# Kernel optimization log

Measured on AMD Instinct MI355X. Metric: run time of the kernel, lower is better.

The kernel has to match this reference:

```python
import jax, jax.numpy as jnp
import numpy as np

NUM_EXPERTS = 8
TOP_K = 2


def setup_inputs() -> dict:
    key = jax.random.key(0)
    ks = jax.random.split(key, 6)
    B, S, D, H, E = 4, 1024, 1024, 2048, NUM_EXPERTS
    x = jax.random.normal(ks[0], (B, S, D), dtype=jnp.float32)
    Wg = jax.random.normal(ks[1], (D, E), dtype=jnp.float32) * 0.02
    W1 = jax.random.normal(ks[2], (E, D, H), dtype=jnp.float32) * 0.02
    b1 = jax.random.normal(ks[3], (E, H), dtype=jnp.float32) * 0.02
    W2 = jax.random.normal(ks[4], (E, H, D), dtype=jnp.float32) * 0.02
    b2 = jax.random.normal(ks[5], (E, D), dtype=jnp.float32) * 0.02
    return {"x": x, "Wg": Wg, "W1": W1, "b1": b1, "W2": W2, "b2": b2}


def reference(x, Wg, W1, b1, W2, b2):
    B, S, D = x.shape
    E, _, H = W1.shape
    OUT = W2.shape[2]
    xm = x.reshape(-1, D)                      # [N, D], N = B*S
    # --- top-k gating (ProbabilitySamplerTopk): softmax over experts, take top-k ---
    logits = xm @ Wg                           # [N, E]
    probs = jax.nn.softmax(logits, axis=-1)
    topk_p, topk_i = jax.lax.top_k(probs, TOP_K)   # [N, K]
    # --- sort dispatched (token, expert) pairs by expert id (stable) ---
    flat_e = topk_i.reshape(-1)                # [N*K]
    flat_p = topk_p.reshape(-1)                # [N*K]
    order = jnp.argsort(flat_e)                # stable sort -> grouped by expert
    tok_idx = order // TOP_K                   # source token index (trunc-div by topK)
    e_sorted = flat_e[order]                   # [N*K]
    p_sorted = flat_p[order]                   # [N*K]
    xs = xm[tok_idx]                           # [N*K, D] expert-sorted inputs
    # --- grouped-GEMM experts: masked per-expert dense GEMM (E is small & fixed) ---
    y = jnp.zeros((xs.shape[0], OUT), dtype=xs.dtype)
    for e in range(E):
        h = jax.nn.relu(xs @ W1[e] + b1[e])    # [N*K, H]
        ye = h @ W2[e] + b2[e]                 # [N*K, OUT]
        m = (e_sorted == e)[:, None].astype(xs.dtype)
        y = y + m * ye
    # --- combine: multiply by gates, scatter-add back to token slots ---
    y = y * p_sorted[:, None]
    out = jnp.zeros((B * S, OUT), dtype=y.dtype).at[tok_idx].add(y)
    return out.reshape(B, S, OUT)
```

## Files before the change

### kernel.cpp

```cpp
#include <hip/hip_runtime.h>
#include <hip/hip_bf16.h>
#include <stdint.h>

typedef __bf16 bf16;
typedef __bf16 bf16x8 __attribute__((ext_vector_type(8)));
typedef __bf16 bf16x4 __attribute__((ext_vector_type(4)));
typedef float f32x4 __attribute__((ext_vector_type(4)));

#define N_TOK 4096
#define DDIM 1024
#define HDIM 2048
#define NPAIR 8192
#define BM 128
#define BN 128
#define BK 32
#define MTILES 71

__device__ __forceinline__ void gload16(const void* g, void* l) {
  __builtin_amdgcn_global_load_lds(
      (const __attribute__((address_space(1))) unsigned int*)g,
      (__attribute__((address_space(3))) unsigned int*)l, 16, 0, 0);
}

__global__ void transpose_cvt_kernel(const float* __restrict__ in, bf16* __restrict__ out,
                                     int R, int C) {
  __shared__ float tile[32][33];
  const float* ip = in + (size_t)blockIdx.z * R * C;
  bf16* op = out + (size_t)blockIdx.z * R * C;
  int r0 = blockIdx.y * 32, c0 = blockIdx.x * 32;
  int tr = threadIdx.x >> 3;
  int tc = (threadIdx.x & 7) * 4;
  float4 v = *(const float4*)(ip + (size_t)(r0 + tr) * C + c0 + tc);
  tile[tr][tc] = v.x; tile[tr][tc + 1] = v.y; tile[tr][tc + 2] = v.z; tile[tr][tc + 3] = v.w;
  __syncthreads();
  bf16x4 o = {(bf16)tile[tc + 0][tr], (bf16)tile[tc + 1][tr],
              (bf16)tile[tc + 2][tr], (bf16)tile[tc + 3][tr]};
  *(bf16x4*)(op + (size_t)(c0 + tr) * R + r0 + tc) = o;
}

__global__ void gate_kernel(const float* __restrict__ x, const float* __restrict__ Wg,
                            int2* __restrict__ ge, float2* __restrict__ gp,
                            bf16* __restrict__ xb) {
  int t = blockIdx.x * 4 + (threadIdx.x >> 6);
  int lane = threadIdx.x & 63;
  const float* xr = x + (size_t)t * DDIM;
  bf16* xbr = xb + (size_t)t * DDIM;
  float a[8];
#pragma unroll
  for (int e = 0; e < 8; e++) a[e] = 0.f;
#pragma unroll
  for (int it = 0; it < 4; it++) {
    int d0 = it * 256 + lane * 4;
    float4 xv = *(const float4*)(xr + d0);
    bf16x4 o = {(bf16)xv.x, (bf16)xv.y, (bf16)xv.z, (bf16)xv.w};
    *(bf16x4*)(xbr + d0) = o;
    float xs[4] = {xv.x, xv.y, xv.z, xv.w};
#pragma unroll
    for (int dd = 0; dd < 4; dd++) {
      float4 w0 = *(const float4*)(Wg + (size_t)(d0 + dd) * 8);
      float4 w1 = *(const float4*)(Wg + (size_t)(d0 + dd) * 8 + 4);
      a[0] += xs[dd] * w0.x; a[1] += xs[dd] * w0.y; a[2] += xs[dd] * w0.z; a[3] += xs[dd] * w0.w;
      a[4] += xs[dd] * w1.x; a[5] += xs[dd] * w1.y; a[6] += xs[dd] * w1.z; a[7] += xs[dd] * w1.w;
    }
  }
#pragma unroll
  for (int off = 32; off >= 1; off >>= 1) {
#pragma unroll
    for (int e = 0; e < 8; e++) a[e] += __shfl_xor(a[e], off);
  }
  if (lane == 0) {
    float m = a[0];
#pragma unroll
    for (int e = 1; e < 8; e++) m = fmaxf(m, a[e]);
    float p[8]; float s = 0.f;
#pragma unroll
    for (int e = 0; e < 8; e++) { p[e] = expf(a[e] - m); s += p[e]; }
    float inv = 1.f / s;
    int i0 = 0; float v0 = a[0];
#pragma unroll
    for (int e = 1; e < 8; e++) if (a[e] > v0) { v0 = a[e]; i0 = e; }
    int i1 = -1; float v1 = -1e30f;
#pragma unroll
    for (int e = 0; e < 8; e++) if (e != i0 && a[e] > v1) { v1 = a[e]; i1 = e; }
    ge[t] = make_int2(i0, i1);
    gp[t] = make_float2(p[i0] * inv, p[i1] * inv);
  }
}

__global__ void sort_kernel(const int2* __restrict__ ge, const float2* __restrict__ gp,
                            int* __restrict__ tok, float* __restrict__ ps,
                            int* __restrict__ pairpos, int* __restrict__ meta) {
  __shared__ int hist[8], runn[8], wc[16][8], wb[16][8], baseS[9];
  int tid = threadIdx.x;
  int lane = tid & 63, wv = tid >> 6;
  if (tid < 8) hist[tid] = 0;
  __syncthreads();
  for (int i = tid; i < NPAIR; i += 1024) {
    int2 g = ge[i >> 1];
    int e = (i & 1) ? g.y : g.x;
    atomicAdd(&hist[e], 1);
  }
  __syncthreads();
  if (tid == 0) {
    int b = 0, ts = 0;
    for (int e = 0; e < 8; e++) {
      baseS[e] = b; meta[e] = b; meta[9 + e] = ts;
      b += hist[e]; ts += (hist[e] + BM - 1) / BM;
    }
    baseS[8] = b; meta[8] = b; meta[17] = ts;
  }
  __syncthreads();
  if (tid < 8) runn[tid] = baseS[tid];
  __syncthreads();
  for (int c = 0; c < 8; c++) {
    int i = c * 1024 + tid;
    int2 g = ge[i >> 1];
    int e = (i & 1) ? g.y : g.x;
    int rank = 0;
#pragma unroll
    for (int ee = 0; ee < 8; ee++) {
      unsigned long long b = __ballot(e == ee);
      if (e == ee) rank = __popcll(b & ((1ull << lane) - 1ull));
      if (lane == 0) wc[wv][ee] = __popcll(b);
    }
    __syncthreads();
    if (tid < 8) {
      int s = runn[tid];
      for (int w = 0; w < 16; w++) { wb[w][tid] = s; s += wc[w][tid]; }
      runn[tid] = s;
    }
    __syncthreads();
    int pos = wb[wv][e] + rank;
    tok[pos] = i >> 1;
    float2 p2 = gp[i >> 1];
    ps[pos] = (i & 1) ? p2.y : p2.x;
    pairpos[i] = pos;
    __syncthreads();
  }
}

template <int KDIM, int NPE, bool FIRST>
__global__ __launch_bounds__(256, 3)
void moe_gemm_kernel(const bf16* __restrict__ A, const bf16* __restrict__ Bt,
                     const float* __restrict__ bias, const int* __restrict__ tok,
                     const float* __restrict__ ps, const int* __restrict__ meta,
                     bf16* __restrict__ hout, float* __restrict__ y2, int MT) {
  __shared__ bf16 lds[3][8192];

  int nwg = gridDim.x;
  int orig = blockIdx.x;
  int q = nwg >> 3, rr8 = nwg & 7;
  int xcd = orig & 7, off8 = orig >> 3;
  int lin = (xcd < rr8 ? xcd * (q + 1) : rr8 * (q + 1) + (xcd - rr8) * q) + off8;
  int tileN = lin / MT;
  int tileM = lin - tileN * MT;
  if (tileM >= meta[17]) return;
  int e = 0;
#pragma unroll
  for (int k = 1; k < 8; k++) if (tileM >= meta[9 + k]) e = k;
  int row0 = meta[e] + (tileM - meta[9 + e]) * BM;
  int segEnd = meta[e + 1];
  int n0 = tileN * BN;

  int t = threadIdx.x;
  const bf16* aSrc[2];
  const bf16* bSrc[2];
#pragma unroll
  for (int r = 0; r < 2; r++) {
    int row = r * 64 + (t >> 2);
    int gRow = row0 + row; if (gRow > NPAIR - 1) gRow = NPAIR - 1;
    int arow = FIRST ? tok[gRow] : gRow;
    int gcol = ((t & 3) ^ ((row >> 1) & 3)) * 8;
    aSrc[r] = A + (size_t)arow * KDIM + gcol;
    bSrc[r] = Bt + ((size_t)e * NPE + n0 + row) * KDIM + gcol;
  }

  int lane = t & 63, wv = t >> 6;
  int wm = wv >> 1, wn = wv & 1;
  int l15 = lane & 15, l4 = lane >> 4;
  int aOff[4], bOff[4];
#pragma unroll
  for (int m = 0; m < 4; m++) {
    int row = wm * 64 + m * 16 + l15;
    aOff[m] = row * 32 + ((l4 ^ ((row >> 1) & 3)) * 8);
  }
#pragma unroll
  for (int n = 0; n < 4; n++) {
    int row = wn * 64 + n * 16 + l15;
    bOff[n] = 4096 + row * 32 + ((l4 ^ ((row >> 1) & 3)) * 8);
  }

  f32x4 acc[4][4];
#pragma unroll
  for (int m = 0; m < 4; m++)
#pragma unroll
    for (int n = 0; n < 4; n++)
#pragma unroll
      for (int j = 0; j < 4; j++) acc[m][n][j] = 0.f;

  auto STAGE = [&](int kt, int slot) {
    bf16* sb = &lds[slot][0];
    int ko = kt * BK;
    gload16(aSrc[0] + ko, sb + t * 8);
    gload16(aSrc[1] + ko, sb + 2048 + t * 8);
    gload16(bSrc[0] + ko, sb + 4096 + t * 8);
    gload16(bSrc[1] + ko, sb + 6144 + t * 8);
  };

  constexpr int nk = KDIM / BK;
  STAGE(0, 0);
  STAGE(1, 1);
  for (int kt = 0; kt < nk; kt++) {
    if (kt == nk - 1) asm volatile("s_waitcnt vmcnt(0)\n\ts_barrier" ::: "memory");
    else              asm volatile("s_waitcnt vmcnt(4)\n\ts_barrier" ::: "memory");
    if (kt + 2 < nk) STAGE(kt + 2, (kt + 2) % 3);
    __builtin_amdgcn_sched_barrier(0);
    const bf16* sb = &lds[kt % 3][0];
    bf16x8 af[4], bfr[4];
#pragma unroll
    for (int m = 0; m < 4; m++) af[m] = *(const bf16x8*)(sb + aOff[m]);
#pragma unroll
    for (int n = 0; n < 4; n++) bfr[n] = *(const bf16x8*)(sb + bOff[n]);
    __builtin_amdgcn_s_setprio(1);
#pragma unroll
    for (int m = 0; m < 4; m++)
#pragma unroll
      for (int n = 0; n < 4; n++)
        acc[m][n] = __builtin_amdgcn_mfma_f32_16x16x32_bf16(af[m], bfr[n], acc[m][n], 0, 0, 0);
    __builtin_amdgcn_s_setprio(0);
  }

  int colb = n0 + wn * 64 + l15;
  int rowb = wm * 64 + l4 * 4;
  float bia[4];
#pragma unroll
  for (int n = 0; n < 4; n++) bia[n] = bias[(size_t)e * NPE + colb + n * 16];
#pragma unroll
  for (int m = 0; m < 4; m++) {
#pragma unroll
    for (int j = 0; j < 4; j++) {
      int gRow = row0 + rowb + m * 16 + j;
      if (gRow < segEnd) {
        if (FIRST) {
#pragma unroll
          for (int n = 0; n < 4; n++) {
            float v = acc[m][n][j] + bia[n];
            v = fmaxf(v, 0.f);
            hout[(size_t)gRow * NPE + colb + n * 16] = (bf16)v;
          }
        } else {
          float pscale = ps[gRow];
#pragma unroll
          for (int n = 0; n < 4; n++) {
            float v = (acc[m][n][j] + bia[n]) * pscale;
            y2[(size_t)gRow * NPE + colb + n * 16] = v;
          }
        }
      }
    }
  }
}

__global__ void combine_kernel(const float* __restrict__ y2, const int* __restrict__ pairpos,
                               float* __restrict__ out) {
  int gi = blockIdx.x * 256 + threadIdx.x;
  int tk = gi >> 8;
  int c4 = (gi & 255) * 4;
  int p0 = pairpos[tk * 2], p1 = pairpos[tk * 2 + 1];
  float4 a = *(const float4*)(y2 + (size_t)p0 * DDIM + c4);
  float4 b = *(const float4*)(y2 + (size_t)p1 * DDIM + c4);
  float4 o = {a.x + b.x, a.y + b.y, a.z + b.z, a.w + b.w};
  *(float4*)(out + (size_t)tk * DDIM + c4) = o;
}

extern "C" void kernel_launch(void* const* d_in, const int* in_sizes, int n_in,
                              void* d_out, int out_size, void* d_ws, size_t ws_size,
                              hipStream_t stream) {
  (void)in_sizes; (void)n_in; (void)out_size; (void)ws_size;
  const float* x  = (const float*)d_in[0];
  const float* Wg = (const float*)d_in[1];
  const float* W1 = (const float*)d_in[2];
  const float* b1 = (const float*)d_in[3];
  const float* W2 = (const float*)d_in[4];
  const float* b2 = (const float*)d_in[5];
  float* out = (float*)d_out;

  char* ws = (char*)d_ws;
  bf16*  xb   = (bf16*)(ws);
  bf16*  W1T  = (bf16*)(ws + (8ull  << 20));
  bf16*  W2T  = (bf16*)(ws + (40ull << 20));
  bf16*  hbuf = (bf16*)(ws + (72ull << 20));
  float* y2   = (float*)(ws + (104ull << 20));
  char*  ext  = ws + (136ull << 20);
  int2*   ge      = (int2*)(ext);
  float2* gp      = (float2*)(ext + (64u  << 10));
  int*    tok     = (int*)(ext + (128u << 10));
  float*  psarr   = (float*)(ext + (160u << 10));
  int*    pairpos = (int*)(ext + (192u << 10));
  int*    meta    = (int*)(ext + (224u << 10));

  transpose_cvt_kernel<<<dim3(64, 32, 8), 256, 0, stream>>>(W1, W1T, 1024, 2048);
  transpose_cvt_kernel<<<dim3(32, 64, 8), 256, 0, stream>>>(W2, W2T, 2048, 1024);
  gate_kernel<<<1024, 256, 0, stream>>>(x, Wg, ge, gp, xb);
  sort_kernel<<<1, 1024, 0, stream>>>(ge, gp, tok, psarr, pairpos, meta);
  moe_gemm_kernel<1024, 2048, true><<<dim3(MTILES * 16), 256, 0, stream>>>(
      xb, W1T, b1, tok, psarr, meta, hbuf, nullptr, MTILES);
  moe_gemm_kernel<2048, 1024, false><<<dim3(MTILES * 8), 256, 0, stream>>>(
      hbuf, W2T, b2, tok, psarr, meta, nullptr, y2, MTILES);
  combine_kernel<<<4096, 256, 0, stream>>>(y2, pairpos, out);
}
```

Measured before the change: 208.8 us.

## Enlarge MoE GEMM M-tile to 256 and fuse combine via atomic scatter-add

The M tile of the grouped expert GEMMs doubles to 256 rows, run by 512-thread workgroups with 8 waves, a larger LDS stage and a single B load per thread. The aim is to raise weight reuse per tile and cut the number of tiles. The second GEMM now atomically adds its gate-scaled results straight into the zeroed output at each token's row. That removes the y2 intermediate buffer, the pairpos array and the separate combine pass. In exchange it adds a zeroing kernel, fp32 global atomics, and more padded rows per expert segment.

Result: slower. 219.1 us (+4.9%).

```diff
diff --git a/kernel.cpp b/kernel.cpp
--- a/kernel.cpp
+++ b/kernel.cpp
@@ -11,10 +11,10 @@
 #define DDIM 1024
 #define HDIM 2048
 #define NPAIR 8192
-#define BM 128
+#define BM 256
 #define BN 128
 #define BK 32
-#define MTILES 71
+#define MTILES 39
 
 __device__ __forceinline__ void gload16(const void* g, void* l) {
   __builtin_amdgcn_global_load_lds(
@@ -89,7 +89,7 @@
 
 __global__ void sort_kernel(const int2* __restrict__ ge, const float2* __restrict__ gp,
                             int* __restrict__ tok, float* __restrict__ ps,
-                            int* __restrict__ pairpos, int* __restrict__ meta) {
+                            int* __restrict__ meta) {
   __shared__ int hist[8], runn[8], wc[16][8], wb[16][8], baseS[9];
   int tid = threadIdx.x;
   int lane = tid & 63, wv = tid >> 6;
@@ -134,18 +134,21 @@
     tok[pos] = i >> 1;
     float2 p2 = gp[i >> 1];
     ps[pos] = (i & 1) ? p2.y : p2.x;
-    pairpos[i] = pos;
     __syncthreads();
   }
 }
 
+__global__ void zero_kernel(float4* __restrict__ p) {
+  p[blockIdx.x * 256 + threadIdx.x] = make_float4(0.f, 0.f, 0.f, 0.f);
+}
+
 template <int KDIM, int NPE, bool FIRST>
-__global__ __launch_bounds__(256, 3)
+__global__ __launch_bounds__(512, 4)
 void moe_gemm_kernel(const bf16* __restrict__ A, const bf16* __restrict__ Bt,
                      const float* __restrict__ bias, const int* __restrict__ tok,
                      const float* __restrict__ ps, const int* __restrict__ meta,
-                     bf16* __restrict__ hout, float* __restrict__ y2, int MT) {
-  __shared__ bf16 lds[3][8192];
+                     bf16* __restrict__ hout, float* __restrict__ outp, int MT) {
+  __shared__ bf16 lds[3][12288];
 
   int nwg = gridDim.x;
   int orig = blockIdx.x;
@@ -164,15 +167,17 @@
 
   int t = threadIdx.x;
   const bf16* aSrc[2];
-  const bf16* bSrc[2];
-#pragma unroll
-  for (int r = 0; r < 2; r++) {
-    int row = r * 64 + (t >> 2);
-    int gRow = row0 + row; if (gRow > NPAIR - 1) gRow = NPAIR - 1;
-    int arow = FIRST ? tok[gRow] : gRow;
-    int gcol = ((t & 3) ^ ((row >> 1) & 3)) * 8;
-    aSrc[r] = A + (size_t)arow * KDIM + gcol;
-    bSrc[r] = Bt + ((size_t)e * NPE + n0 + row) * KDIM + gcol;
+  const bf16* bSrc;
+  {
+    int swz = ((t & 3) ^ ((t >> 3) & 3)) * 8;
+#pragma unroll
+    for (int r = 0; r < 2; r++) {
+      int row = r * 128 + (t >> 2);
+      int gRow = row0 + row; if (gRow > NPAIR - 1) gRow = NPAIR - 1;
+      int arow = FIRST ? tok[gRow] : gRow;
+      aSrc[r] = A + (size_t)arow * KDIM + swz;
+    }
+    bSrc = Bt + ((size_t)e * NPE + n0 + (t >> 2)) * KDIM + swz;
   }
 
   int lane = t & 63, wv = t >> 6;
@@ -187,7 +192,7 @@
 #pragma unroll
   for (int n = 0; n < 4; n++) {
     int row = wn * 64 + n * 16 + l15;
-    bOff[n] = 4096 + row * 32 + ((l4 ^ ((row >> 1) & 3)) * 8);
+    bOff[n] = 8192 + row * 32 + ((l4 ^ ((row >> 1) & 3)) * 8);
   }
 
   f32x4 acc[4][4];
@@ -202,9 +207,8 @@
     bf16* sb = &lds[slot][0];
     int ko = kt * BK;
     gload16(aSrc[0] + ko, sb + t * 8);
-    gload16(aSrc[1] + ko, sb + 2048 + t * 8);
-    gload16(bSrc[0] + ko, sb + 4096 + t * 8);
-    gload16(bSrc[1] + ko, sb + 6144 + t * 8);
+    gload16(aSrc[1] + ko, sb + 4096 + t * 8);
+    gload16(bSrc + ko, sb + 8192 + t * 8);
   };
 
   constexpr int nk = KDIM / BK;
@@ -212,7 +216,7 @@
   STAGE(1, 1);
   for (int kt = 0; kt < nk; kt++) {
     if (kt == nk - 1) asm volatile("s_waitcnt vmcnt(0)\n\ts_barrier" ::: "memory");
-    else              asm volatile("s_waitcnt vmcnt(4)\n\ts_barrier" ::: "memory");
+    else              asm volatile("s_waitcnt vmcnt(3)\n\ts_barrier" ::: "memory");
     if (kt + 2 < nk) STAGE(kt + 2, (kt + 2) % 3);
     __builtin_amdgcn_sched_barrier(0);
     const bf16* sb = &lds[kt % 3][0];
@@ -250,10 +254,11 @@
           }
         } else {
           float pscale = ps[gRow];
+          float* orow = outp + (size_t)tok[gRow] * DDIM;
 #pragma unroll
           for (int n = 0; n < 4; n++) {
             float v = (acc[m][n][j] + bia[n]) * pscale;
-            y2[(size_t)gRow * NPE + colb + n * 16] = v;
+            atomicAdd(orow + colb + n * 16, v);
           }
         }
       }
@@ -261,22 +266,10 @@
   }
 }
 
-__global__ void combine_kernel(const float* __restrict__ y2, const int* __restrict__ pairpos,
-                               float* __restrict__ out) {
-  int gi = blockIdx.x * 256 + threadIdx.x;
-  int tk = gi >> 8;
-  int c4 = (gi & 255) * 4;
-  int p0 = pairpos[tk * 2], p1 = pairpos[tk * 2 + 1];
-  float4 a = *(const float4*)(y2 + (size_t)p0 * DDIM + c4);
-  float4 b = *(const float4*)(y2 + (size_t)p1 * DDIM + c4);
-  float4 o = {a.x + b.x, a.y + b.y, a.z + b.z, a.w + b.w};
-  *(float4*)(out + (size_t)tk * DDIM + c4) = o;
-}
-
 extern "C" void kernel_launch(void* const* d_in, const int* in_sizes, int n_in,
                               void* d_out, int out_size, void* d_ws, size_t ws_size,
                               hipStream_t stream) {
-  (void)in_sizes; (void)n_in; (void)out_size; (void)ws_size;
+  (void)in_sizes; (void)n_in; (void)ws_size;
   const float* x  = (const float*)d_in[0];
   const float* Wg = (const float*)d_in[1];
   const float* W1 = (const float*)d_in[2];
@@ -290,22 +283,20 @@
   bf16*  W1T  = (bf16*)(ws + (8ull  << 20));
   bf16*  W2T  = (bf16*)(ws + (40ull << 20));
   bf16*  hbuf = (bf16*)(ws + (72ull << 20));
-  float* y2   = (float*)(ws + (104ull << 20));
-  char*  ext  = ws + (136ull << 20);
+  char*  ext  = ws + (104ull << 20);
   int2*   ge      = (int2*)(ext);
   float2* gp      = (float2*)(ext + (64u  << 10));
   int*    tok     = (int*)(ext + (128u << 10));
   float*  psarr   = (float*)(ext + (160u << 10));
-  int*    pairpos = (int*)(ext + (192u << 10));
   int*    meta    = (int*)(ext + (224u << 10));
 
   transpose_cvt_kernel<<<dim3(64, 32, 8), 256, 0, stream>>>(W1, W1T, 1024, 2048);
   transpose_cvt_kernel<<<dim3(32, 64, 8), 256, 0, stream>>>(W2, W2T, 2048, 1024);
   gate_kernel<<<1024, 256, 0, stream>>>(x, Wg, ge, gp, xb);
-  sort_kernel<<<1, 1024, 0, stream>>>(ge, gp, tok, psarr, pairpos, meta);
-  moe_gemm_kernel<1024, 2048, true><<<dim3(MTILES * 16), 256, 0, stream>>>(
+  sort_kernel<<<1, 1024, 0, stream>>>(ge, gp, tok, psarr, meta);
+  zero_kernel<<<out_size / 1024, 256, 0, stream>>>((float4*)out);
+  moe_gemm_kernel<1024, 2048, true><<<dim3(MTILES * 16), 512, 0, stream>>>(
       xb, W1T, b1, tok, psarr, meta, hbuf, nullptr, MTILES);
-  moe_gemm_kernel<2048, 1024, false><<<dim3(MTILES * 8), 256, 0, stream>>>(
-      hbuf, W2T, b2, tok, psarr, meta, nullptr, y2, MTILES);
-  combine_kernel<<<4096, 256, 0, stream>>>(y2, pairpos, out);
-}
+  moe_gemm_kernel<2048, 1024, false><<<dim3(MTILES * 8), 512, 0, stream>>>(
+      hbuf, W2T, b2, tok, psarr, meta, nullptr, out, MTILES);
+}
```
